# Performance work log

Measured on AMD Instinct MI355X. Metric: run time of the kernel, lower is better.

The kernel has to match this reference:

```python
import jax, jax.numpy as jnp
import numpy as np

N, C, H, W = 8, 64, 64, 64
K = C // 8  # 8 channels for f/g projections


def setup_inputs() -> dict:
    key = jax.random.key(0)
    ks = jax.random.split(key, 8)
    return {
        "inputs": jax.random.normal(ks[0], (N, C, H, W), dtype=jnp.float32),
        "Wf": jax.random.normal(ks[1], (K, C), dtype=jnp.float32) * 0.05,
        "bf": jax.random.normal(ks[2], (K,), dtype=jnp.float32) * 0.05,
        "Wg": jax.random.normal(ks[3], (K, C), dtype=jnp.float32) * 0.05,
        "bg": jax.random.normal(ks[4], (K,), dtype=jnp.float32) * 0.05,
        "Ws": jax.random.normal(ks[5], (1, C), dtype=jnp.float32) * 0.05,
        "bs": jax.random.normal(ks[6], (1,), dtype=jnp.float32) * 0.05,
        "gamma": jax.random.normal(ks[7], (1,), dtype=jnp.float32),
    }


def reference(inputs, Wf, bf, Wg, bg, Ws, bs, gamma):
    n, c, h, w = inputs.shape
    hw = h * w
    x = inputs.reshape(n, c, hw)                       # [N, C, HW]
    # 1x1 convs == per-pixel linear projections
    f = jnp.einsum('kc,ncp->nkp', Wf, x) + bf[None, :, None]   # [N, K, HW]
    g = jnp.einsum('kc,ncp->nkp', Wg, x) + bg[None, :, None]   # [N, K, HW]
    s = jnp.einsum('kc,ncp->nkp', Ws, x) + bs[None, :, None]   # [N, 1, HW]
    # attention scores over all spatial positions
    beta = jnp.einsum('nkp,nkq->npq', f, g)            # [N, HW, HW]
    beta = jax.nn.softmax(beta, axis=-1)
    # attention map: weighted sum of the 1-channel s projection
    att = jnp.einsum('npq,nq->np', beta, s[:, 0, :])   # [N, HW]
    att_map = att.reshape(n, 1, h, w)
    output = att_map * gamma[0] + inputs
    return (att_map, output)
```

## Files before the change

### kernel.cpp

```cpp
#include <hip/hip_runtime.h>

#define NB 8
#define CH 64
#define KP 8
#define HWP 4096
#define NHW (NB * HWP)
#define PTILE 64
#define QC 512
#define NCHUNK (HWP / QC)

typedef float f32x16 __attribute__((ext_vector_type(16)));
typedef __bf16 bf16x8 __attribute__((ext_vector_type(8)));
typedef short short8v __attribute__((ext_vector_type(8)));

#define WS_FB  0
#define WS_GB  (NHW * 4)
#define WS_SB  (NHW * 8)

__device__ __forceinline__ int s_shuf_idx(int i) {
    return i ^ (((((i >> 2) ^ (i >> 3)) & 1) != 0) ? 12 : 0);
}

__global__ __launch_bounds__(512) void proj_kernel(
    const float* __restrict__ x,
    const float* __restrict__ Wf, const float* __restrict__ bf,
    const float* __restrict__ Wg, const float* __restrict__ bg,
    const float* __restrict__ Ws, const float* __restrict__ bs,
    float* __restrict__ ws)
{
    __shared__ float part[3][128][17];

    const int blk = blockIdx.x;
    const int n   = blk >> 5;
    const int p0  = (blk & 31) << 7;
    const int px  = threadIdx.x & 127;
    const int q   = threadIdx.x >> 7;
    const int p   = p0 + px;

    const float* xp = x + (size_t)n * CH * HWP + (size_t)(q * 16) * HWP + p;

    float accf[KP], accg[KP], accs;
    if (q == 0) {
#pragma unroll
        for (int k = 0; k < KP; ++k) { accf[k] = bf[k]; accg[k] = bg[k]; }
        accs = bs[0];
    } else {
#pragma unroll
        for (int k = 0; k < KP; ++k) { accf[k] = 0.f; accg[k] = 0.f; }
        accs = 0.f;
    }

#pragma unroll
    for (int c = 0; c < 16; ++c) {
        float xv = xp[(size_t)c * HWP];
        int cc = q * 16 + c;
#pragma unroll
        for (int k = 0; k < KP; ++k) {
            accf[k] = fmaf(Wf[k * CH + cc], xv, accf[k]);
            accg[k] = fmaf(Wg[k * CH + cc], xv, accg[k]);
        }
        accs = fmaf(Ws[cc], xv, accs);
    }

    if (q != 0) {
        float* dst = part[q - 1][px];
#pragma unroll
        for (int k = 0; k < KP; ++k) { dst[k] = accf[k]; dst[KP + k] = accg[k]; }
        dst[16] = accs;
    }
    __syncthreads();

    if (q == 0) {
#pragma unroll
        for (int j = 0; j < 3; ++j) {
            const float* src = part[j][px];
#pragma unroll
            for (int k = 0; k < KP; ++k) { accf[k] += src[k]; accg[k] += src[KP + k]; }
            accs += src[16];
        }

        const float L2E = 1.4426950408889634f;
        bf16x8 fv, gv;
#pragma unroll
        for (int k = 0; k < KP; ++k) {
            fv[k] = (__bf16)(accf[k] * L2E);
            gv[k] = (__bf16)accg[k];
        }

        ushort* fb = (ushort*)(ws + WS_FB) + (size_t)(n * HWP + p) * 8;
        ushort* gb = (ushort*)(ws + WS_GB) + (size_t)(n * HWP + p) * 8;
        *(short8v*)fb = __builtin_bit_cast(short8v, fv);
        *(short8v*)gb = __builtin_bit_cast(short8v, gv);

        __bf16 sb16 = (__bf16)accs;
        ((ushort*)(ws + WS_SB))[(size_t)n * HWP + (p & ~15) + s_shuf_idx(p & 15)] =
            __builtin_bit_cast(ushort, sb16);
    }
}

__global__ __launch_bounds__(512, 8) void attn_finish_kernel(
    const float* __restrict__ x, const float* __restrict__ gamma,
    float* __restrict__ ws, float* __restrict__ out)
{
    __shared__ alignas(16) ushort g_lds[2][(QC + 1) * KP];
    __shared__ alignas(16) ushort s_lds[2][QC];
    __shared__ ushort ones_lds[32];
    __shared__ float  part_l[4][PTILE];
    __shared__ float  part_a[4][PTILE];
    __shared__ float  att_lds[PTILE];

    const int blk  = blockIdx.x;
    const int n    = blk >> 6;
    const int p0   = (blk & 63) << 6;
    const int tid  = threadIdx.x;
    const int lane = tid & 63;
    const int w    = tid >> 6;
    const int pg   = w & 1;
    const int qs   = w >> 1;
    const int l31  = lane & 31;
    const int hi   = lane >> 5;

    if (tid < 16) ((uint*)ones_lds)[tid] = 0x3F803F80u;
    if (tid < 8) { g_lds[0][QC * KP + tid] = 0; g_lds[1][QC * KP + tid] = 0; }

    const ushort* fbase = (const ushort*)(ws + WS_FB) + (size_t)n * HWP * KP;
    short8v z8 = {0, 0, 0, 0, 0, 0, 0, 0};
    bf16x8 bfrag = __builtin_bit_cast(bf16x8,
        hi ? z8 : *(const short8v*)(fbase + (size_t)(p0 + pg * 32 + l31) * KP));

    const float4* gsrc = (const float4*)((const ushort*)(ws + WS_GB) +
                                         (size_t)n * HWP * KP);
    const float4* ssrc = (const float4*)((const ushort*)(ws + WS_SB) +
                                         (size_t)n * HWP);

    const f32x16 czero = {0.f};
    f32x16 c_pv = {0.f};

    ((float4*)g_lds[0])[tid] = gsrc[tid];
    if (tid < QC / 8) ((float4*)s_lds[0])[tid] = ssrc[tid];
    __syncthreads();

#pragma unroll 1
    for (int j = 0; j < NCHUNK; ++j) {
        const int buf = j & 1;
        if (j + 1 < NCHUNK) {
            ((float4*)g_lds[buf ^ 1])[tid] = gsrc[(j + 1) * QC + tid];
            if (tid < QC / 8)
                ((float4*)s_lds[buf ^ 1])[tid] = ssrc[(j + 1) * (QC / 8) + tid];
        }
        const ushort* gb = g_lds[buf];
        const ushort* sb = s_lds[buf];

#pragma unroll 1
        for (int t = 0; t < 4; ++t) {
            const int ql = qs * 128 + t * 32;
            int arow = hi ? QC : (ql + l31);
            bf16x8 afrag = __builtin_bit_cast(bf16x8,
                *(const short8v*)(gb + (size_t)arow * KP));

            f32x16 c = __builtin_amdgcn_mfma_f32_32x32x16_bf16(
                afrag, bfrag, czero, 0, 0, 0);
#pragma unroll
            for (int r = 0; r < 16; ++r) c[r] = __builtin_amdgcn_exp2f(c[r]);

            bf16x8 elo, ehi;
#pragma unroll
            for (int r = 0; r < 8; ++r) { elo[r] = (__bf16)c[r]; ehi[r] = (__bf16)c[r + 8]; }

            const ushort* ap = (l31 == 1) ? ones_lds : (sb + ql + (hi << 3));
            bf16x8 a1 = __builtin_bit_cast(bf16x8, *(const short8v*)ap);
            bf16x8 a2 = __builtin_bit_cast(bf16x8, *(const short8v*)(ap + 16));

            c_pv = __builtin_amdgcn_mfma_f32_32x32x16_bf16(a1, elo, c_pv, 0, 0, 0);
            c_pv = __builtin_amdgcn_mfma_f32_32x32x16_bf16(a2, ehi, c_pv, 0, 0, 0);
        }
        __syncthreads();
    }

    if (!hi) {
        part_a[qs][pg * 32 + l31] = c_pv[0];
        part_l[qs][pg * 32 + l31] = c_pv[1];
    }
    __syncthreads();

    if (tid < PTILE) {
        float l = (part_l[0][tid] + part_l[1][tid]) + (part_l[2][tid] + part_l[3][tid]);
        float a = (part_a[0][tid] + part_a[1][tid]) + (part_a[2][tid] + part_a[3][tid]);
        float att = a / l;
        att_lds[tid] = att;
        out[(size_t)n * HWP + p0 + tid] = att;
    }
    __syncthreads();

    const float gm = gamma[0];
    const float* xn = x + (size_t)n * CH * HWP + p0;
    float* outp = out + NHW + (size_t)n * CH * HWP + p0;
#pragma unroll
    for (int it = 0; it < 2; ++it) {
        int idx = it * 512 + tid;
        int c   = idx >> 4;
        int p4  = (idx & 15) << 2;
        float4 xv = *(const float4*)(xn + (size_t)c * HWP + p4);
        float4 av = *(const float4*)(att_lds + p4);
        float4 o;
        o.x = fmaf(av.x, gm, xv.x);
        o.y = fmaf(av.y, gm, xv.y);
        o.z = fmaf(av.z, gm, xv.z);
        o.w = fmaf(av.w, gm, xv.w);
        *(float4*)(outp + (size_t)c * HWP + p4) = o;
    }
}

extern "C" void kernel_launch(void* const* d_in, const int* in_sizes, int n_in,
                              void* d_out, int out_size, void* d_ws, size_t ws_size,
                              hipStream_t stream) {
    const float* x     = (const float*)d_in[0];
    const float* Wf    = (const float*)d_in[1];
    const float* bf    = (const float*)d_in[2];
    const float* Wg    = (const float*)d_in[3];
    const float* bg    = (const float*)d_in[4];
    const float* Ws    = (const float*)d_in[5];
    const float* bs    = (const float*)d_in[6];
    const float* gamma = (const float*)d_in[7];
    float* out = (float*)d_out;
    float* ws  = (float*)d_ws;

    proj_kernel<<<NB * (HWP / 128), 512, 0, stream>>>(x, Wf, bf, Wg, bg, Ws, bs, ws);
    attn_finish_kernel<<<NB * (HWP / PTILE), 512, 0, stream>>>(x, gamma, ws, out);
}
```

Baseline: 30.58 us.

## Load g fragments directly from global with register prefetch, stage all of s in LDS

Replaces the double-buffered LDS staging of g and s chunks, which needed a block-wide barrier per chunk, with per-wave direct global loads of the g fragment. Each load is software-prefetched one iteration ahead into registers. The whole per-batch s vector is loaded into LDS once up front, and each wave pair now walks a contiguous 1024-key range with no in-loop synchronisation. This removes eight __syncthreads and the cooperative LDS copies. The cost is that the g fragment loads now go through global/L2 latency rather than LDS, and each wave fetches its own rows with no sharing across waves.

```diff
diff --git a/kernel.cpp b/kernel.cpp
--- a/kernel.cpp
+++ b/kernel.cpp
@@ -6,8 +6,6 @@
 #define HWP 4096
 #define NHW (NB * HWP)
 #define PTILE 64
-#define QC 512
-#define NCHUNK (HWP / QC)
 
 typedef float f32x16 __attribute__((ext_vector_type(16)));
 typedef __bf16 bf16x8 __attribute__((ext_vector_type(8)));
@@ -102,8 +100,7 @@
     const float* __restrict__ x, const float* __restrict__ gamma,
     float* __restrict__ ws, float* __restrict__ out)
 {
-    __shared__ alignas(16) ushort g_lds[2][(QC + 1) * KP];
-    __shared__ alignas(16) ushort s_lds[2][QC];
+    __shared__ alignas(16) ushort s_lds[HWP];
     __shared__ ushort ones_lds[32];
     __shared__ float  part_l[4][PTILE];
     __shared__ float  part_a[4][PTILE];
@@ -120,61 +117,48 @@
     const int l31  = lane & 31;
     const int hi   = lane >> 5;
 
+    ((float4*)s_lds)[tid] =
+        ((const float4*)((const ushort*)(ws + WS_SB) + (size_t)n * HWP))[tid];
     if (tid < 16) ((uint*)ones_lds)[tid] = 0x3F803F80u;
-    if (tid < 8) { g_lds[0][QC * KP + tid] = 0; g_lds[1][QC * KP + tid] = 0; }
 
     const ushort* fbase = (const ushort*)(ws + WS_FB) + (size_t)n * HWP * KP;
     short8v z8 = {0, 0, 0, 0, 0, 0, 0, 0};
     bf16x8 bfrag = __builtin_bit_cast(bf16x8,
         hi ? z8 : *(const short8v*)(fbase + (size_t)(p0 + pg * 32 + l31) * KP));
 
-    const float4* gsrc = (const float4*)((const ushort*)(ws + WS_GB) +
-                                         (size_t)n * HWP * KP);
-    const float4* ssrc = (const float4*)((const ushort*)(ws + WS_SB) +
-                                         (size_t)n * HWP);
+    const ushort* gbase = (const ushort*)(ws + WS_GB) + (size_t)n * HWP * KP;
+
+    __syncthreads();
 
     const f32x16 czero = {0.f};
     f32x16 c_pv = {0.f};
 
-    ((float4*)g_lds[0])[tid] = gsrc[tid];
-    if (tid < QC / 8) ((float4*)s_lds[0])[tid] = ssrc[tid];
-    __syncthreads();
+    const int qw = qs << 10;
+    short8v araw = z8;
+    if (!hi) araw = *(const short8v*)(gbase + (size_t)(qw + l31) * KP);
 
 #pragma unroll 1
-    for (int j = 0; j < NCHUNK; ++j) {
-        const int buf = j & 1;
-        if (j + 1 < NCHUNK) {
-            ((float4*)g_lds[buf ^ 1])[tid] = gsrc[(j + 1) * QC + tid];
-            if (tid < QC / 8)
-                ((float4*)s_lds[buf ^ 1])[tid] = ssrc[(j + 1) * (QC / 8) + tid];
-        }
-        const ushort* gb = g_lds[buf];
-        const ushort* sb = s_lds[buf];
-
-#pragma unroll 1
-        for (int t = 0; t < 4; ++t) {
-            const int ql = qs * 128 + t * 32;
-            int arow = hi ? QC : (ql + l31);
-            bf16x8 afrag = __builtin_bit_cast(bf16x8,
-                *(const short8v*)(gb + (size_t)arow * KP));
-
-            f32x16 c = __builtin_amdgcn_mfma_f32_32x32x16_bf16(
-                afrag, bfrag, czero, 0, 0, 0);
-#pragma unroll
-            for (int r = 0; r < 16; ++r) c[r] = __builtin_amdgcn_exp2f(c[r]);
-
-            bf16x8 elo, ehi;
-#pragma unroll
-            for (int r = 0; r < 8; ++r) { elo[r] = (__bf16)c[r]; ehi[r] = (__bf16)c[r + 8]; }
-
-            const ushort* ap = (l31 == 1) ? ones_lds : (sb + ql + (hi << 3));
-            bf16x8 a1 = __builtin_bit_cast(bf16x8, *(const short8v*)ap);
-            bf16x8 a2 = __builtin_bit_cast(bf16x8, *(const short8v*)(ap + 16));
-
-            c_pv = __builtin_amdgcn_mfma_f32_32x32x16_bf16(a1, elo, c_pv, 0, 0, 0);
-            c_pv = __builtin_amdgcn_mfma_f32_32x32x16_bf16(a2, ehi, c_pv, 0, 0, 0);
-        }
-        __syncthreads();
+    for (int t = 0; t < 32; ++t) {
+        bf16x8 afrag = __builtin_bit_cast(bf16x8, araw);
+        if (t + 1 < 32 && !hi)
+            araw = *(const short8v*)(gbase + (size_t)(qw + (t + 1) * 32 + l31) * KP);
+
+        f32x16 c = __builtin_amdgcn_mfma_f32_32x32x16_bf16(
+            afrag, bfrag, czero, 0, 0, 0);
+#pragma unroll
+        for (int r = 0; r < 16; ++r) c[r] = __builtin_amdgcn_exp2f(c[r]);
+
+        bf16x8 elo, ehi;
+#pragma unroll
+        for (int r = 0; r < 8; ++r) { elo[r] = (__bf16)c[r]; ehi[r] = (__bf16)c[r + 8]; }
+
+        const int qbase = qw + (t << 5);
+        const ushort* ap = (l31 == 1) ? ones_lds : (s_lds + qbase + (hi << 3));
+        bf16x8 a1 = __builtin_bit_cast(bf16x8, *(const short8v*)ap);
+        bf16x8 a2 = __builtin_bit_cast(bf16x8, *(const short8v*)(ap + 16));
+
+        c_pv = __builtin_amdgcn_mfma_f32_32x32x16_bf16(a1, elo, c_pv, 0, 0, 0);
+        c_pv = __builtin_amdgcn_mfma_f32_32x32x16_bf16(a2, ehi, c_pv, 0, 0, 0);
     }
 
     if (!hi) {
```

Result: no change. 30.28 us (-1.0%).
